# Kernel optimization log

Measured on AMD Instinct MI355X. Metric: run time of the kernel, lower is better.

Reference implementation:

```python
import jax, jax.numpy as jnp
import numpy as np

B, S, D, H, W = 2, 4096, 1024, 8, 1024  # batch, seq, model_dim, heads, window
DH = D // H
EPS = 1e-5


def setup_inputs() -> dict:
    key = jax.random.key(0)
    ks = jax.random.split(key, 4)
    scale = 0.02
    return {
        "val": jax.random.normal(ks[0], (B, S, D), dtype=jnp.float32),
        "w_qkv": jax.random.normal(ks[1], (D, 3 * D), dtype=jnp.float32) * scale,
        "b_qkv": jnp.zeros((3 * D,), dtype=jnp.float32),
        "w_out": jax.random.normal(ks[2], (D, D), dtype=jnp.float32) * scale,
        "b_out": jnp.zeros((D,), dtype=jnp.float32),
        "ln_gamma": jnp.ones((D,), dtype=jnp.float32),
        "ln_beta": jnp.zeros((D,), dtype=jnp.float32),
    }


def _layer_norm(x, gamma, beta):
    mu = jnp.mean(x, axis=-1, keepdims=True)
    var = jnp.mean(jnp.square(x - mu), axis=-1, keepdims=True)
    return (x - mu) * jax.lax.rsqrt(var + EPS) * gamma + beta


def reference(val, w_qkv, b_qkv, w_out, b_out, ln_gamma, ln_beta):
    nb = S // W  # number of local windows
    qkv = val @ w_qkv + b_qkv                       # [B, S, 3D]
    qkv = qkv.reshape(B, nb, W, 3, H, DH)
    q, k, v = qkv[..., 0, :, :], qkv[..., 1, :, :], qkv[..., 2, :, :]  # [B,nb,W,H,DH]
    scores = jnp.einsum("bnwhd,bnxhd->bnhwx", q, k) / jnp.sqrt(jnp.float32(DH))
    attn = jax.nn.softmax(scores, axis=-1)          # [B,nb,H,W,W]
    ctx = jnp.einsum("bnhwx,bnxhd->bnwhd", attn, v).reshape(B, S, D)
    attn_out = ctx @ w_out + b_out                  # [B,S,D]
    return _layer_norm(val + attn_out, ln_gamma, ln_beta)
```

## Files before the change

kernel.cpp:

```cpp
#include <hip/hip_runtime.h>
#include <hip/hip_bf16.h>
#include <stdint.h>


typedef float f32x4 __attribute__((ext_vector_type(4)));
typedef __bf16 bf16x8 __attribute__((ext_vector_type(8)));

static __device__ __forceinline__ unsigned short f2bf(float f) {
    unsigned int u = __builtin_bit_cast(unsigned int, f);
    u += 0x7fffu + ((u >> 16) & 1u);
    return (unsigned short)(u >> 16);
}

static __device__ __forceinline__ unsigned cvt_pk_bf16(float lo, float hi) {
    unsigned r;
    asm("v_cvt_pk_bf16_f32 %0, %1, %2" : "=v"(r) : "v"(lo), "v"(hi));
    return r;
}

static __device__ __forceinline__ void gload_lds16(const void* g, void* l) {
    __builtin_amdgcn_global_load_lds(
        (__attribute__((address_space(1))) void*)(g),
        (__attribute__((address_space(3))) void*)(l), 16, 0, 0);
}

#define VMCNT(n) asm volatile("s_waitcnt vmcnt(" #n ")" ::: "memory")

__global__ __launch_bounds__(256) void k_convert(const float* __restrict__ in,
                                                 unsigned short* __restrict__ out,
                                                 int n4) {
    int i = blockIdx.x * 256 + threadIdx.x;
    if (i >= n4) return;
    float4 v = ((const float4*)in)[i];
    ushort4 o;
    o.x = f2bf(v.x); o.y = f2bf(v.y); o.z = f2bf(v.z); o.w = f2bf(v.w);
    ((ushort4*)out)[i] = o;
}

__global__ __launch_bounds__(256) void k_transpose(const float* __restrict__ in,
                                                   unsigned short* __restrict__ out,
                                                   int R, int C) {
    __shared__ float tile[64][65];
    const int rt = blockIdx.y * 64, ct = blockIdx.x * 64;
    const int t = threadIdx.x;
#pragma unroll
    for (int i = 0; i < 4; ++i) {
        int fid = i * 256 + t;
        int r = fid >> 4;
        int c = (fid & 15) << 2;
        float4 v = *(const float4*)&in[(size_t)(rt + r) * C + ct + c];
        tile[r][c] = v.x; tile[r][c + 1] = v.y; tile[r][c + 2] = v.z; tile[r][c + 3] = v.w;
    }
    __syncthreads();
#pragma unroll
    for (int i = 0; i < 4; ++i) {
        int fid = i * 256 + t;
        int c = fid >> 4;
        int r0 = (fid & 15) << 2;
        ushort4 o;
        o.x = f2bf(tile[r0][c]);     o.y = f2bf(tile[r0 + 1][c]);
        o.z = f2bf(tile[r0 + 2][c]); o.w = f2bf(tile[r0 + 3][c]);
        *(ushort4*)&out[(size_t)(ct + c) * R + rt + r0] = o;
    }
}

template <int MODE>
__global__ __launch_bounds__(256, 2) void k_gemm(
    const unsigned short* __restrict__ A,
    const unsigned short* __restrict__ Bt,
    const float* __restrict__ bias,
    const float* __restrict__ resid,
    unsigned short* __restrict__ out_qk,
    unsigned short* __restrict__ out_vT,
    float* __restrict__ out_f,
    int Kdim)
{
    __shared__ __align__(16) unsigned short Al[128 * 64];
    __shared__ __align__(16) unsigned short Bl[128 * 64];
    const int t = threadIdx.x;
    const int wave = t >> 6, lane = t & 63;
    const int wm = wave >> 1, wn = wave & 1;
    const int lr = lane & 15, lg = lane >> 4;
    const int tile_m = blockIdx.y * 128;
    const int tile_n = blockIdx.x * 128;

    f32x4 acc[4][4];
#pragma unroll
    for (int i = 0; i < 4; ++i)
#pragma unroll
        for (int j = 0; j < 4; ++j)
            acc[i][j] = (f32x4){0.f, 0.f, 0.f, 0.f};

    const int srow = lane >> 3;
    const int scol = (lane & 7) * 8;

    for (int kt = 0; kt < Kdim; kt += 64) {
#pragma unroll
        for (int i = 0; i < 4; ++i) {
            int chunk = i * 4 + wave;
            int row = chunk * 8 + srow;
            gload_lds16(&A[(size_t)(tile_m + row) * Kdim + kt + scol], &Al[chunk * 512]);
            gload_lds16(&Bt[(size_t)(tile_n + row) * Kdim + kt + scol], &Bl[chunk * 512]);
        }
        __syncthreads();
#pragma unroll
        for (int kk = 0; kk < 2; ++kk) {
            bf16x8 af[4], bfr[4];
#pragma unroll
            for (int mi = 0; mi < 4; ++mi)
                af[mi] = *(const bf16x8*)&Al[(wm * 64 + mi * 16 + lr) * 64 + kk * 32 + lg * 8];
#pragma unroll
            for (int ni = 0; ni < 4; ++ni)
                bfr[ni] = *(const bf16x8*)&Bl[(wn * 64 + ni * 16 + lr) * 64 + kk * 32 + lg * 8];
#pragma unroll
            for (int mi = 0; mi < 4; ++mi)
#pragma unroll
                for (int ni = 0; ni < 4; ++ni)
                    acc[mi][ni] = __builtin_amdgcn_mfma_f32_16x16x32_bf16(af[mi], bfr[ni], acc[mi][ni], 0, 0, 0);
        }
        __syncthreads();
    }

#pragma unroll
    for (int ni = 0; ni < 4; ++ni) {
        int n = tile_n + wn * 64 + ni * 16 + lr;
        float bv = bias[n];
#pragma unroll
        for (int mi = 0; mi < 4; ++mi) {
            int m0 = tile_m + wm * 64 + mi * 16 + lg * 4;
            f32x4 v = acc[mi][ni];
            if (MODE == 0) {
                if (n < 2048) {
#pragma unroll
                    for (int r = 0; r < 4; ++r)
                        out_qk[(size_t)(m0 + r) * 2048 + n] = f2bf(v[r] + bv);
                } else {
                    int hd = (n - 2048) >> 7;
                    int dd = (n - 2048) & 127;
                    int bn = m0 >> 10;
                    int x0 = m0 & 1023;
                    ushort4 o;
                    o.x = f2bf(v[0] + bv); o.y = f2bf(v[1] + bv);
                    o.z = f2bf(v[2] + bv); o.w = f2bf(v[3] + bv);
                    *(ushort4*)&out_vT[((size_t)(bn * 8 + hd) * 128 + dd) * 1024 + x0] = o;
                }
            } else {
#pragma unroll
                for (int r = 0; r < 4; ++r) {
                    size_t idx = (size_t)(m0 + r) * 1024 + n;
                    out_f[idx] = v[r] + bv + resid[idx];
                }
            }
        }
    }
}

__global__ __launch_bounds__(256, 2) void k_attn(
    const unsigned short* __restrict__ qk,
    const unsigned short* __restrict__ vT,
    unsigned short* __restrict__ ctx)
{
    __shared__ __align__(16) unsigned short Kl[2 * 64 * 128];
    __shared__ __align__(16) unsigned short Vl[2 * 128 * 64];
    __shared__ __align__(16) unsigned short Pl[128 * 64];
    const int t = threadIdx.x;
    const int wave = t >> 6, lane = t & 63;
    const int lr = lane & 15, lg = lane >> 4;

    const int lid = blockIdx.y * gridDim.x + blockIdx.x;
    const int xcd = lid & 7, slot = lid >> 3;
    const int head = xcd * 8 + (slot & 7);
    const int qblk = slot >> 3;

    const int h = head & 7;
    const int tok0 = (head >> 3) * 1024;
    const int qtok = tok0 + qblk * 128 + wave * 32;
    const float cl2 = 0.08838834764831845f * 1.44269504088896f;

    const unsigned short* kbase = &qk[(size_t)tok0 * 2048 + 1024 + h * 128];
    const unsigned short* vhead = &vT[(size_t)head * 128 * 1024];

    auto stage = [&](int x0, int buf) {
        unsigned short* Kb = (unsigned short*)((char*)Kl + buf * 16384);
        unsigned short* Vb = (unsigned short*)((char*)Vl + buf * 16384);
#pragma unroll
        for (int i = 0; i < 4; ++i) {
            int x = i * 16 + wave * 4 + (lane >> 4);
            int ck = (lane & 15) ^ (x & 7);
            gload_lds16(&kbase[(size_t)(x0 + x) * 2048 + ck * 8], &Kb[i * 2048 + wave * 512]);
            int d = i * 32 + wave * 8 + (lane >> 3);
            int cv = (lane & 7) ^ (d & 7);
            gload_lds16(&vhead[(size_t)d * 1024 + x0 + cv * 8], &Vb[i * 2048 + wave * 512]);
        }
    };

    bf16x8 qf[2][4];
#pragma unroll
    for (int nq = 0; nq < 2; ++nq)
#pragma unroll
        for (int kk = 0; kk < 4; ++kk)
            qf[nq][kk] = *(const bf16x8*)&qk[(size_t)(qtok + 16 * nq + lr) * 2048 + h * 128 + kk * 32 + lg * 8];

    f32x4 o[2][8];
#pragma unroll
    for (int a = 0; a < 2; ++a)
#pragma unroll
        for (int b = 0; b < 8; ++b)
            o[a][b] = (f32x4){0.f, 0.f, 0.f, 0.f};
    float m_run[2] = {-3.0e38f, -3.0e38f};
    float l_run[2] = {0.f, 0.f};

    stage(0, 0);

    for (int tile = 0; tile < 16; ++tile) {
        const int kb = (tile & 1) * 16384;
        if (tile < 15) {
            stage((tile + 1) * 64, (tile + 1) & 1);
            VMCNT(8);
        } else {
            VMCNT(0);
        }
        __builtin_amdgcn_sched_barrier(0);
        __builtin_amdgcn_s_barrier();
        __builtin_amdgcn_sched_barrier(0);

        f32x4 s[4][2];
#pragma unroll
        for (int mi = 0; mi < 4; ++mi)
#pragma unroll
            for (int nq = 0; nq < 2; ++nq)
                s[mi][nq] = (f32x4){0.f, 0.f, 0.f, 0.f};
#pragma unroll
        for (int kk = 0; kk < 4; ++kk) {
            bf16x8 kf[4];
#pragma unroll
            for (int mi = 0; mi < 4; ++mi) {
                int row = mi * 16 + lr;
                int byte = (row * 256 + kk * 64 + lg * 16) ^ ((row & 7) << 4);
                kf[mi] = *(const bf16x8*)((const char*)Kl + kb + byte);
            }
            __builtin_amdgcn_s_setprio(1);
#pragma unroll
            for (int mi = 0; mi < 4; ++mi)
#pragma unroll
                for (int nq = 0; nq < 2; ++nq)
                    s[mi][nq] = __builtin_amdgcn_mfma_f32_16x16x32_bf16(kf[mi], qf[nq][kk], s[mi][nq], 0, 0, 0);
            __builtin_amdgcn_s_setprio(0);
        }

        float fac[2];
        bool doresc[2];
#pragma unroll
        for (int nq = 0; nq < 2; ++nq) {
            float mx = -3.0e38f;
#pragma unroll
            for (int mi = 0; mi < 4; ++mi)
#pragma unroll
                for (int r = 0; r < 4; ++r)
                    mx = fmaxf(mx, s[mi][nq][r]);
            mx = fmaxf(mx, __shfl_xor(mx, 16));
            mx = fmaxf(mx, __shfl_xor(mx, 32));
            float mxl = mx * cl2;
            float mr = m_run[nq];
            if (__any(mxl - mr > 8.0f)) {
                float mn = fmaxf(mr, mxl);
                fac[nq] = __builtin_amdgcn_exp2f(mr - mn);
                m_run[nq] = mn;
                doresc[nq] = true;
            } else {
                fac[nq] = 1.0f;
                doresc[nq] = false;
            }
            const float nmn = -m_run[nq];
            float sum = 0.f;
            const int q = wave * 32 + nq * 16 + lr;
#pragma unroll
            for (int mi = 0; mi < 4; ++mi) {
                float p0 = __builtin_amdgcn_exp2f(__builtin_fmaf(s[mi][nq][0], cl2, nmn));
                float p1 = __builtin_amdgcn_exp2f(__builtin_fmaf(s[mi][nq][1], cl2, nmn));
                float p2 = __builtin_amdgcn_exp2f(__builtin_fmaf(s[mi][nq][2], cl2, nmn));
                float p3 = __builtin_amdgcn_exp2f(__builtin_fmaf(s[mi][nq][3], cl2, nmn));
                sum += (p0 + p1) + (p2 + p3);
                uint2 pk;
                pk.x = cvt_pk_bf16(p0, p1);
                pk.y = cvt_pk_bf16(p2, p3);
                int byte = (q * 128 + (mi * 16 + lg * 4) * 2) ^ ((q & 7) << 4);
                *(uint2*)((char*)Pl + byte) = pk;
            }
            sum += __shfl_xor(sum, 16);
            sum += __shfl_xor(sum, 32);
            l_run[nq] = l_run[nq] * fac[nq] + sum;
        }

#pragma unroll
        for (int mo = 0; mo < 2; ++mo)
            if (doresc[mo]) {
#pragma unroll
                for (int r = 0; r < 4; ++r) {
                    int src = (lane & 48) | (lg * 4 + r);
                    float f = __shfl(fac[mo], src);
#pragma unroll
                    for (int nd = 0; nd < 8; ++nd)
                        o[mo][nd][r] *= f;
                }
            }

#pragma unroll
        for (int kk = 0; kk < 2; ++kk) {
            bf16x8 pf[2], vf[8];
#pragma unroll
            for (int mo = 0; mo < 2; ++mo) {
                int q = wave * 32 + mo * 16 + lr;
                int byte = (q * 128 + kk * 64 + lg * 16) ^ ((q & 7) << 4);
                pf[mo] = *(const bf16x8*)((const char*)Pl + byte);
            }
#pragma unroll
            for (int nd = 0; nd < 8; ++nd) {
                int drow = nd * 16 + lr;
                int byte = (drow * 128 + kk * 64 + lg * 16) ^ ((drow & 7) << 4);
                vf[nd] = *(const bf16x8*)((const char*)Vl + kb + byte);
            }
            __builtin_amdgcn_s_setprio(1);
#pragma unroll
            for (int mo = 0; mo < 2; ++mo)
#pragma unroll
                for (int nd = 0; nd < 8; ++nd)
                    o[mo][nd] = __builtin_amdgcn_mfma_f32_16x16x32_bf16(pf[mo], vf[nd], o[mo][nd], 0, 0, 0);
            __builtin_amdgcn_s_setprio(0);
        }
        __builtin_amdgcn_s_barrier();
        __builtin_amdgcn_sched_barrier(0);
    }

#pragma unroll
    for (int mo = 0; mo < 2; ++mo) {
        float rl[4];
#pragma unroll
        for (int r = 0; r < 4; ++r) {
            int src = (lane & 48) | (lg * 4 + r);
            rl[r] = 1.0f / __shfl(l_run[mo], src);
        }
#pragma unroll
        for (int nd = 0; nd < 8; ++nd)
#pragma unroll
            for (int r = 0; r < 4; ++r) {
                int q = qtok + mo * 16 + lg * 4 + r;
                ctx[(size_t)q * 1024 + h * 128 + nd * 16 + lr] = f2bf(o[mo][nd][r] * rl[r]);
            }
    }
}

__global__ __launch_bounds__(256) void k_ln(float* __restrict__ io,
                                            const float* __restrict__ gamma,
                                            const float* __restrict__ beta)
{
    __shared__ float bs[4], bss[4];
    const int row = blockIdx.x;
    const int t = threadIdx.x;
    float4 v = ((const float4*)&io[(size_t)row * 1024])[t];
    float s = (v.x + v.y) + (v.z + v.w);
    float ss = (v.x * v.x + v.y * v.y) + (v.z * v.z + v.w * v.w);
#pragma unroll
    for (int off = 32; off >= 1; off >>= 1) {
        s += __shfl_xor(s, off);
        ss += __shfl_xor(ss, off);
    }
    if ((t & 63) == 0) { bs[t >> 6] = s; bss[t >> 6] = ss; }
    __syncthreads();
    s = (bs[0] + bs[1]) + (bs[2] + bs[3]);
    ss = (bss[0] + bss[1]) + (bss[2] + bss[3]);
    const float mu = s * (1.f / 1024.f);
    const float var = ss * (1.f / 1024.f) - mu * mu;
    const float rs = rsqrtf(var + 1e-5f);
    float4 g = ((const float4*)gamma)[t];
    float4 b = ((const float4*)beta)[t];
    float4 ov;
    ov.x = (v.x - mu) * rs * g.x + b.x;
    ov.y = (v.y - mu) * rs * g.y + b.y;
    ov.z = (v.z - mu) * rs * g.z + b.z;
    ov.w = (v.w - mu) * rs * g.w + b.w;
    ((float4*)&io[(size_t)row * 1024])[t] = ov;
}

extern "C" void kernel_launch(void* const* d_in, const int* in_sizes, int n_in,
                              void* d_out, int out_size, void* d_ws, size_t ws_size,
                              hipStream_t stream)
{
    const float* val   = (const float*)d_in[0];
    const float* w_qkv = (const float*)d_in[1];
    const float* b_qkv = (const float*)d_in[2];
    const float* w_out = (const float*)d_in[3];
    const float* b_out = (const float*)d_in[4];
    const float* ln_g  = (const float*)d_in[5];
    const float* ln_b  = (const float*)d_in[6];
    float* out = (float*)d_out;

    char* ws = (char*)d_ws;
    unsigned short* qk     = (unsigned short*)(ws + 0);
    unsigned short* vTb    = (unsigned short*)(ws + 33554432);
    unsigned short* ctx    = (unsigned short*)(ws + 50331648);
    unsigned short* w_outT = (unsigned short*)(ws + 67108864);
    unsigned short* w_qkvT = (unsigned short*)(ws + 69206016);
    unsigned short* valb   = (unsigned short*)(ws + 75497472);

    k_convert<<<8192, 256, 0, stream>>>(val, valb, 2097152);
    k_transpose<<<dim3(48, 16), 256, 0, stream>>>(w_qkv, w_qkvT, 1024, 3072);
    k_transpose<<<dim3(16, 16), 256, 0, stream>>>(w_out, w_outT, 1024, 1024);
    k_gemm<0><<<dim3(24, 64), 256, 0, stream>>>(valb, w_qkvT, b_qkv, nullptr, qk, vTb, nullptr, 1024);
    k_attn<<<dim3(8, 64), 256, 0, stream>>>(qk, vTb, ctx);
    k_gemm<1><<<dim3(8, 64), 256, 0, stream>>>(ctx, w_outT, b_out, val, nullptr, nullptr, out, 1024);
    k_ln<<<8192, 256, 0, stream>>>(out, ln_g, ln_b);
}
```

Measured before the change: 175.8 us.

## Rewrite QKV GEMM with 256x256 tiles, 8 waves, and double-buffered async LDS loads

Result: slower. 182.0 us (+3.5%).

```diff
diff --git a/kernel.cpp b/kernel.cpp
--- a/kernel.cpp
+++ b/kernel.cpp
@@ -25,6 +25,7 @@
 }
 
 #define VMCNT(n) asm volatile("s_waitcnt vmcnt(" #n ")" ::: "memory")
+#define SB() __builtin_amdgcn_sched_barrier(0)
 
 __global__ __launch_bounds__(256) void k_convert(const float* __restrict__ in,
                                                  unsigned short* __restrict__ out,
@@ -64,14 +65,149 @@
     }
 }
 
-template <int MODE>
-__global__ __launch_bounds__(256, 2) void k_gemm(
+__global__ __launch_bounds__(512, 2) void k_gemm1(
+    const unsigned short* __restrict__ A,
+    const unsigned short* __restrict__ Bt,
+    const float* __restrict__ bias,
+    unsigned short* __restrict__ out_qk,
+    unsigned short* __restrict__ out_vT)
+{
+    __shared__ __align__(16) char smem[131072];
+    const int t = threadIdx.x;
+    const int wave = t >> 6, lane = t & 63;
+    const int lr = lane & 15, lg = lane >> 4;
+    const int wr = wave >> 2, wc = wave & 3;
+
+    const int lid = blockIdx.x;
+    const int swz = (lid & 7) * 48 + (lid >> 3);
+    const int tile_m = (swz / 12) * 256;
+    const int tile_n = (swz % 12) * 256;
+
+    const int srow8 = lane >> 3;
+    const int sblk = (lane & 7) ^ srow8;
+
+    f32x4 acc[8][4];
+#pragma unroll
+    for (int i = 0; i < 8; ++i)
+#pragma unroll
+        for (int j = 0; j < 4; ++j)
+            acc[i][j] = (f32x4){0.f, 0.f, 0.f, 0.f};
+
+    auto stage2 = [&](int kt, int buf, int h) {
+#pragma unroll
+        for (int i = 0; i < 2; ++i) {
+            int r = i * 64 + wave * 8 + srow8;
+            int dst = buf * 32768 + h * 16384 + (i * 512 + wave * 64) * 16;
+            gload_lds16(&A[(size_t)(tile_m + h * 128 + r) * 1024 + kt * 64 + sblk * 8],
+                        smem + dst);
+            gload_lds16(&Bt[(size_t)(tile_n + h * 128 + r) * 1024 + kt * 64 + sblk * 8],
+                        smem + 65536 + dst);
+        }
+    };
+
+    stage2(0, 0, 0);
+    stage2(0, 0, 1);
+    VMCNT(0);
+    SB(); __builtin_amdgcn_s_barrier(); SB();
+
+    bf16x8 af[4][2], bf0[2][2], bf1[2][2];
+
+    for (int tt = 0; tt < 8; ++tt) {
+#pragma unroll
+        for (int p = 0; p < 8; ++p) {
+            const int b = p >> 2, q = p & 3;
+            const int mh = q >> 1, nh = q & 1;
+            const int abase = b * 32768;
+            const int bbase = 65536 + b * 32768;
+            if (nh == 0) {
+#pragma unroll
+                for (int mi = 0; mi < 4; ++mi) {
+                    const int row = wr * 128 + mh * 64 + mi * 16 + lr;
+#pragma unroll
+                    for (int kk = 0; kk < 2; ++kk)
+                        af[mi][kk] = *(const bf16x8*)(smem + abase + row * 128 +
+                                        (((kk * 4 + lg) ^ (row & 7)) << 4));
+                }
+            }
+            if (q == 0) {
+#pragma unroll
+                for (int ni = 0; ni < 2; ++ni) {
+                    const int row = wc * 64 + ni * 16 + lr;
+#pragma unroll
+                    for (int kk = 0; kk < 2; ++kk)
+                        bf0[ni][kk] = *(const bf16x8*)(smem + bbase + row * 128 +
+                                        (((kk * 4 + lg) ^ (row & 7)) << 4));
+                }
+            }
+            if (q == 1) {
+#pragma unroll
+                for (int ni = 0; ni < 2; ++ni) {
+                    const int row = wc * 64 + 32 + ni * 16 + lr;
+#pragma unroll
+                    for (int kk = 0; kk < 2; ++kk)
+                        bf1[ni][kk] = *(const bf16x8*)(smem + bbase + row * 128 +
+                                        (((kk * 4 + lg) ^ (row & 7)) << 4));
+                }
+            }
+            if (p == 0) stage2(2 * tt + 1, 1, 0);
+            if (p == 1) stage2(2 * tt + 1, 1, 1);
+            if (p == 4 && tt < 7) stage2(2 * tt + 2, 0, 0);
+            if (p == 5 && tt < 7) stage2(2 * tt + 2, 0, 1);
+
+            SB(); __builtin_amdgcn_s_barrier(); SB();
+
+            __builtin_amdgcn_s_setprio(1);
+#pragma unroll
+            for (int kk = 0; kk < 2; ++kk)
+#pragma unroll
+                for (int mi = 0; mi < 4; ++mi)
+#pragma unroll
+                    for (int ni = 0; ni < 2; ++ni) {
+                        if (nh == 0)
+                            acc[mh * 4 + mi][ni] = __builtin_amdgcn_mfma_f32_16x16x32_bf16(
+                                af[mi][kk], bf0[ni][kk], acc[mh * 4 + mi][ni], 0, 0, 0);
+                        else
+                            acc[mh * 4 + mi][2 + ni] = __builtin_amdgcn_mfma_f32_16x16x32_bf16(
+                                af[mi][kk], bf1[ni][kk], acc[mh * 4 + mi][2 + ni], 0, 0, 0);
+                    }
+            __builtin_amdgcn_s_setprio(0);
+
+            if (q == 3) { VMCNT(0); }
+            SB(); __builtin_amdgcn_s_barrier(); SB();
+        }
+    }
+
+#pragma unroll
+    for (int J = 0; J < 4; ++J) {
+        const int n = tile_n + wc * 64 + (J >> 1) * 32 + (J & 1) * 16 + lr;
+        const float bv = bias[n];
+#pragma unroll
+        for (int I = 0; I < 8; ++I) {
+            const int m0 = tile_m + wr * 128 + (I >> 2) * 64 + (I & 3) * 16 + lg * 4;
+            f32x4 v = acc[I][J];
+            if (n < 2048) {
+#pragma unroll
+                for (int r = 0; r < 4; ++r)
+                    out_qk[(size_t)(m0 + r) * 2048 + n] = f2bf(v[r] + bv);
+            } else {
+                int hd = (n - 2048) >> 7;
+                int dd = (n - 2048) & 127;
+                int bn = m0 >> 10;
+                int x0 = m0 & 1023;
+                ushort4 o;
+                o.x = f2bf(v[0] + bv); o.y = f2bf(v[1] + bv);
+                o.z = f2bf(v[2] + bv); o.w = f2bf(v[3] + bv);
+                *(ushort4*)&out_vT[((size_t)(bn * 8 + hd) * 128 + dd) * 1024 + x0] = o;
+            }
+        }
+    }
+}
+
+__global__ __launch_bounds__(256, 2) void k_gemm2(
     const unsigned short* __restrict__ A,
     const unsigned short* __restrict__ Bt,
     const float* __restrict__ bias,
     const float* __restrict__ resid,
-    unsigned short* __restrict__ out_qk,
-    unsigned short* __restrict__ out_vT,
     float* __restrict__ out_f,
     int Kdim)
 {
@@ -129,27 +265,10 @@
         for (int mi = 0; mi < 4; ++mi) {
             int m0 = tile_m + wm * 64 + mi * 16 + lg * 4;
             f32x4 v = acc[mi][ni];
-            if (MODE == 0) {
-                if (n < 2048) {
-#pragma unroll
-                    for (int r = 0; r < 4; ++r)
-                        out_qk[(size_t)(m0 + r) * 2048 + n] = f2bf(v[r] + bv);
-                } else {
-                    int hd = (n - 2048) >> 7;
-                    int dd = (n - 2048) & 127;
-                    int bn = m0 >> 10;
-                    int x0 = m0 & 1023;
-                    ushort4 o;
-                    o.x = f2bf(v[0] + bv); o.y = f2bf(v[1] + bv);
-                    o.z = f2bf(v[2] + bv); o.w = f2bf(v[3] + bv);
-                    *(ushort4*)&out_vT[((size_t)(bn * 8 + hd) * 128 + dd) * 1024 + x0] = o;
-                }
-            } else {
-#pragma unroll
-                for (int r = 0; r < 4; ++r) {
-                    size_t idx = (size_t)(m0 + r) * 1024 + n;
-                    out_f[idx] = v[r] + bv + resid[idx];
-                }
+#pragma unroll
+            for (int r = 0; r < 4; ++r) {
+                size_t idx = (size_t)(m0 + r) * 1024 + n;
+                out_f[idx] = v[r] + bv + resid[idx];
             }
         }
     }
@@ -220,9 +339,7 @@
         } else {
             VMCNT(0);
         }
-        __builtin_amdgcn_sched_barrier(0);
-        __builtin_amdgcn_s_barrier();
-        __builtin_amdgcn_sched_barrier(0);
+        SB(); __builtin_amdgcn_s_barrier(); SB();
 
         f32x4 s[4][2];
 #pragma unroll
@@ -328,8 +445,7 @@
                     o[mo][nd] = __builtin_amdgcn_mfma_f32_16x16x32_bf16(pf[mo], vf[nd], o[mo][nd], 0, 0, 0);
             __builtin_amdgcn_s_setprio(0);
         }
-        __builtin_amdgcn_s_barrier();
-        __builtin_amdgcn_sched_barrier(0);
+        __builtin_amdgcn_s_barrier(); SB();
     }
 
 #pragma unroll
@@ -406,8 +522,8 @@
     k_convert<<<8192, 256, 0, stream>>>(val, valb, 2097152);
     k_transpose<<<dim3(48, 16), 256, 0, stream>>>(w_qkv, w_qkvT, 1024, 3072);
     k_transpose<<<dim3(16, 16), 256, 0, stream>>>(w_out, w_outT, 1024, 1024);
-    k_gemm<0><<<dim3(24, 64), 256, 0, stream>>>(valb, w_qkvT, b_qkv, nullptr, qk, vTb, nullptr, 1024);
+    k_gemm1<<<384, 512, 0, stream>>>(valb, w_qkvT, b_qkv, qk, vTb);
     k_attn<<<dim3(8, 64), 256, 0, stream>>>(qk, vTb, ctx);
-    k_gemm<1><<<dim3(8, 64), 256, 0, stream>>>(ctx, w_outT, b_out, val, nullptr, nullptr, out, 1024);
+    k_gemm2<<<dim3(8, 64), 256, 0, stream>>>(ctx, w_outT, b_out, val, out, 1024);
     k_ln<<<8192, 256, 0, stream>>>(out, ln_g, ln_b);
 }
```

## Restructure GEMM into 256x128 tiles with triple-buffered async LDS pipeline

Applied to the files above, without the earlier changes.

Measured after the change: 155.4 us (median of 2 runs). -11.6%, faster.

```diff
diff --git a/kernel.cpp b/kernel.cpp
--- a/kernel.cpp
+++ b/kernel.cpp
@@ -25,6 +25,7 @@
 }
 
 #define VMCNT(n) asm volatile("s_waitcnt vmcnt(" #n ")" ::: "memory")
+#define SB() __builtin_amdgcn_sched_barrier(0)
 
 __global__ __launch_bounds__(256) void k_convert(const float* __restrict__ in,
                                                  unsigned short* __restrict__ out,
@@ -64,25 +65,29 @@
     }
 }
 
-template <int MODE>
-__global__ __launch_bounds__(256, 2) void k_gemm(
+template <int MODE, int NTILES>
+__global__ __launch_bounds__(512) void k_gemm(
     const unsigned short* __restrict__ A,
     const unsigned short* __restrict__ Bt,
     const float* __restrict__ bias,
     const float* __restrict__ resid,
     unsigned short* __restrict__ out_qk,
     unsigned short* __restrict__ out_vT,
-    float* __restrict__ out_f,
-    int Kdim)
+    float* __restrict__ out_f)
 {
-    __shared__ __align__(16) unsigned short Al[128 * 64];
-    __shared__ __align__(16) unsigned short Bl[128 * 64];
+    __shared__ __align__(16) char smem[147456];
     const int t = threadIdx.x;
     const int wave = t >> 6, lane = t & 63;
-    const int wm = wave >> 1, wn = wave & 1;
     const int lr = lane & 15, lg = lane >> 4;
-    const int tile_m = blockIdx.y * 128;
-    const int tile_n = blockIdx.x * 128;
+    const int wr = wave >> 1, wc = wave & 1;
+
+    const int lid = blockIdx.x;
+    const int swz = (lid & 7) * (4 * NTILES) + (lid >> 3);
+    const int tile_m = (swz / NTILES) * 256;
+    const int tile_n = (swz % NTILES) * 128;
+
+    const int srow = lane >> 3;
+    const int sblk = (lane & 7) ^ srow;
 
     f32x4 acc[4][4];
 #pragma unroll
@@ -91,44 +96,90 @@
         for (int j = 0; j < 4; ++j)
             acc[i][j] = (f32x4){0.f, 0.f, 0.f, 0.f};
 
-    const int srow = lane >> 3;
-    const int scol = (lane & 7) * 8;
-
-    for (int kt = 0; kt < Kdim; kt += 64) {
-#pragma unroll
-        for (int i = 0; i < 4; ++i) {
-            int chunk = i * 4 + wave;
-            int row = chunk * 8 + srow;
-            gload_lds16(&A[(size_t)(tile_m + row) * Kdim + kt + scol], &Al[chunk * 512]);
-            gload_lds16(&Bt[(size_t)(tile_n + row) * Kdim + kt + scol], &Bl[chunk * 512]);
-        }
-        __syncthreads();
-#pragma unroll
-        for (int kk = 0; kk < 2; ++kk) {
-            bf16x8 af[4], bfr[4];
+    auto stage2 = [&](int kt, int buf, int h) {
+#pragma unroll
+        for (int i = 0; i < 2; ++i) {
+            int r = h * 128 + i * 64 + wave * 8 + srow;
+            int dst = buf * 49152 + h * 16384 + i * 8192 + wave * 1024 + lane * 16;
+            gload_lds16(&A[(size_t)(tile_m + r) * 1024 + kt * 64 + sblk * 8], smem + dst);
+        }
+        int rb = h * 64 + wave * 8 + srow;
+        int dstb = buf * 49152 + 32768 + h * 8192 + wave * 1024 + lane * 16;
+        gload_lds16(&Bt[(size_t)(tile_n + rb) * 1024 + kt * 64 + sblk * 8], smem + dstb);
+    };
+
+    stage2(0, 0, 0); stage2(0, 0, 1);
+    stage2(1, 1, 0); stage2(1, 1, 1);
+
+    bf16x8 af[4][2], bf[2][2];
+
+    for (int kt = 0; kt < 16; ++kt) {
+        const int buf = kt % 3;
+        if (kt == 15) { VMCNT(0); } else { VMCNT(6); }
+        SB(); __builtin_amdgcn_s_barrier(); SB();
+
+        const int abase = buf * 49152;
+        const int bbase = buf * 49152 + 32768;
+
+#pragma unroll
+        for (int mi = 0; mi < 4; ++mi) {
+            const int row = wr * 64 + mi * 16 + lr;
+#pragma unroll
+            for (int kk = 0; kk < 2; ++kk)
+                af[mi][kk] = *(const bf16x8*)(smem + abase + row * 128 +
+                                (((kk * 4 + lg) ^ (row & 7)) << 4));
+        }
+#pragma unroll
+        for (int ni = 0; ni < 2; ++ni) {
+            const int row = wc * 64 + ni * 16 + lr;
+#pragma unroll
+            for (int kk = 0; kk < 2; ++kk)
+                bf[ni][kk] = *(const bf16x8*)(smem + bbase + row * 128 +
+                                (((kk * 4 + lg) ^ (row & 7)) << 4));
+        }
+        if (kt < 14) stage2(kt + 2, (kt + 2) % 3, 0);
+
+        __builtin_amdgcn_s_setprio(1);
+#pragma unroll
+        for (int kk = 0; kk < 2; ++kk)
 #pragma unroll
             for (int mi = 0; mi < 4; ++mi)
-                af[mi] = *(const bf16x8*)&Al[(wm * 64 + mi * 16 + lr) * 64 + kk * 32 + lg * 8];
-#pragma unroll
-            for (int ni = 0; ni < 4; ++ni)
-                bfr[ni] = *(const bf16x8*)&Bl[(wn * 64 + ni * 16 + lr) * 64 + kk * 32 + lg * 8];
+#pragma unroll
+                for (int ni = 0; ni < 2; ++ni)
+                    acc[mi][ni] = __builtin_amdgcn_mfma_f32_16x16x32_bf16(
+                        af[mi][kk], bf[ni][kk], acc[mi][ni], 0, 0, 0);
+        __builtin_amdgcn_s_setprio(0);
+
+#pragma unroll
+        for (int ni = 0; ni < 2; ++ni) {
+            const int row = wc * 64 + 32 + ni * 16 + lr;
+#pragma unroll
+            for (int kk = 0; kk < 2; ++kk)
+                bf[ni][kk] = *(const bf16x8*)(smem + bbase + row * 128 +
+                                (((kk * 4 + lg) ^ (row & 7)) << 4));
+        }
+        if (kt < 14) stage2(kt + 2, (kt + 2) % 3, 1);
+
+        __builtin_amdgcn_s_setprio(1);
+#pragma unroll
+        for (int kk = 0; kk < 2; ++kk)
 #pragma unroll
             for (int mi = 0; mi < 4; ++mi)
 #pragma unroll
-                for (int ni = 0; ni < 4; ++ni)
-                    acc[mi][ni] = __builtin_amdgcn_mfma_f32_16x16x32_bf16(af[mi], bfr[ni], acc[mi][ni], 0, 0, 0);
-        }
-        __syncthreads();
-    }
-
-#pragma unroll
-    for (int ni = 0; ni < 4; ++ni) {
-        int n = tile_n + wn * 64 + ni * 16 + lr;
-        float bv = bias[n];
-#pragma unroll
-        for (int mi = 0; mi < 4; ++mi) {
-            int m0 = tile_m + wm * 64 + mi * 16 + lg * 4;
-            f32x4 v = acc[mi][ni];
+                for (int ni = 0; ni < 2; ++ni)
+                    acc[mi][2 + ni] = __builtin_amdgcn_mfma_f32_16x16x32_bf16(
+                        af[mi][kk], bf[ni][kk], acc[mi][2 + ni], 0, 0, 0);
+        __builtin_amdgcn_s_setprio(0);
+    }
+
+#pragma unroll
+    for (int J = 0; J < 4; ++J) {
+        const int n = tile_n + wc * 64 + J * 16 + lr;
+        const float bv = bias[n];
+#pragma unroll
+        for (int I = 0; I < 4; ++I) {
+            const int m0 = tile_m + wr * 64 + I * 16 + lg * 4;
+            f32x4 v = acc[I][J];
             if (MODE == 0) {
                 if (n < 2048) {
 #pragma unroll
@@ -220,9 +271,7 @@
         } else {
             VMCNT(0);
         }
-        __builtin_amdgcn_sched_barrier(0);
-        __builtin_amdgcn_s_barrier();
-        __builtin_amdgcn_sched_barrier(0);
+        SB(); __builtin_amdgcn_s_barrier(); SB();
 
         f32x4 s[4][2];
 #pragma unroll
@@ -328,8 +377,7 @@
                     o[mo][nd] = __builtin_amdgcn_mfma_f32_16x16x32_bf16(pf[mo], vf[nd], o[mo][nd], 0, 0, 0);
             __builtin_amdgcn_s_setprio(0);
         }
-        __builtin_amdgcn_s_barrier();
-        __builtin_amdgcn_sched_barrier(0);
+        __builtin_amdgcn_s_barrier(); SB();
     }
 
 #pragma unroll
@@ -406,8 +454,8 @@
     k_convert<<<8192, 256, 0, stream>>>(val, valb, 2097152);
     k_transpose<<<dim3(48, 16), 256, 0, stream>>>(w_qkv, w_qkvT, 1024, 3072);
     k_transpose<<<dim3(16, 16), 256, 0, stream>>>(w_out, w_outT, 1024, 1024);
-    k_gemm<0><<<dim3(24, 64), 256, 0, stream>>>(valb, w_qkvT, b_qkv, nullptr, qk, vTb, nullptr, 1024);
+    k_gemm<0, 24><<<768, 512, 0, stream>>>(valb, w_qkvT, b_qkv, nullptr, qk, vTb, nullptr);
     k_attn<<<dim3(8, 64), 256, 0, stream>>>(qk, vTb, ctx);
-    k_gemm<1><<<dim3(8, 64), 256, 0, stream>>>(ctx, w_outT, b_out, val, nullptr, nullptr, out, 1024);
+    k_gemm<1, 8><<<256, 512, 0, stream>>>(ctx, w_outT, b_out, val, nullptr, nullptr, out);
     k_ln<<<8192, 256, 0, stream>>>(out, ln_g, ln_b);
 }
```
